# Kernel tuning notes

Hardware: AMD Instinct MI355X
Metric: run time of the kernel (lower is better)

The kernel has to match this reference:

```python
import jax, jax.numpy as jnp
import numpy as np

N_NODES = 100000
N_EDGES = 1600000
D = 64


def setup_inputs() -> dict:
    key = jax.random.key(0)
    k1, k2, k3, k4 = jax.random.split(key, 4)
    x = jax.random.normal(k1, (N_NODES, D), dtype=jnp.float32)
    # glorot-uniform scale for Linear weight [out_dim, in_dim]
    stdv = np.sqrt(6.0 / (D + D)).astype(np.float32)
    W = jax.random.uniform(k2, (D, D), dtype=jnp.float32, minval=-stdv, maxval=stdv)
    bias = jnp.zeros((D,), dtype=jnp.float32)  # forward() uses a zero bias
    edge_index = jax.random.randint(k3, (2, N_EDGES), 0, N_NODES, dtype=jnp.int64)
    counts = jax.random.randint(k4, (N_NODES,), 0, 16, dtype=jnp.int64)
    out_edge_index = jnp.arange(N_EDGES, dtype=jnp.int64)
    return {"x": x, "W": W, "bias": bias, "edge_index": edge_index,
            "counts": counts, "out_edge_index": out_edge_index, "layer_i": 0}


def reference(x, W, bias, edge_index, counts, out_edge_index, layer_i):
    # GCN layer: y = x @ W^T; gather by source; scatter-sum by destination; add bias.
    # counts / out_edge_index / layer_i are layout hints for the fused CUDA kernel
    # (mygraph.gcn) and do not change the math.
    y = x @ W.T                              # [N, D_out]
    src = edge_index[0]                      # [E]
    dst = edge_index[1]                      # [E]
    msgs = y[src]                            # [E, D_out] edge gather
    out = jax.ops.segment_sum(msgs, dst, num_segments=x.shape[0])  # [N, D_out]
    return out + bias
```

## Files before the change

### kernel.cpp

```cpp
#include <hip/hip_runtime.h>


#define DIM 64
#define BN 64
#define BN_SHIFT 6
#define BN_MASK 63
#define NB_MAX 2048
#define PB 256
#define CAPE 1536
#define OVF_MAX 262144

__device__ __forceinline__ unsigned short f32_to_bf16_rne(float f) {
    unsigned u = __float_as_uint(f);
    unsigned r = u + 0x7FFFu + ((u >> 16) & 1u);
    return (unsigned short)(r >> 16);
}

__global__ __launch_bounds__(1024) void fused_prep_kernel(
        const float* __restrict__ x, const int* __restrict__ ei,
        ushort4* __restrict__ xb4, int* __restrict__ gcnt,
        int* __restrict__ binned, int* __restrict__ ovf,
        int* __restrict__ ovfcnt, int E, int N, int nb, int total4) {
    __shared__ int h[NB_MAX];
    const int t = threadIdx.x;
    const int bid = blockIdx.x;

    for (int b = t; b < nb; b += 1024) h[b] = 0;
    __syncthreads();

    for (int i = bid * 1024 + t; i < total4; i += PB * 1024) {
        float4 v = ((const float4*)x)[i];
        ushort4 o;
        o.x = f32_to_bf16_rne(v.x); o.y = f32_to_bf16_rne(v.y);
        o.z = f32_to_bf16_rne(v.z); o.w = f32_to_bf16_rne(v.w);
        xb4[i] = o;
    }
    if (bid == 0 && t < 16) {
        ushort4 z; z.x = 0; z.y = 0; z.z = 0; z.w = 0;
        xb4[(size_t)N * 16 + t] = z;
    }

    for (int e = bid * 1024 + t; e < E; e += PB * 1024)
        atomicAdd(&h[ei[E + e] >> BN_SHIFT], 1);
    __syncthreads();

    for (int b = t; b < nb; b += 1024) {
        int c = h[b];
        int base = 0;
        if (c > 0) base = atomicAdd(&gcnt[b], c);
        h[b] = b * CAPE + base;
    }
    __syncthreads();

    for (int e = bid * 1024 + t; e < E; e += PB * 1024) {
        int s = ei[e];
        int d = ei[E + e];
        int b = d >> BN_SHIFT;
        int p = atomicAdd(&h[b], 1);
        if (p < b * CAPE + CAPE) {
            binned[p] = (s << BN_SHIFT) | (d & BN_MASK);
        } else {
            int q = atomicAdd(ovfcnt, 1);
            if (q < OVF_MAX) { ovf[2 * q] = s; ovf[2 * q + 1] = d; }
        }
    }
}

__device__ __forceinline__ void acc8(float (&a)[8], const uint4& v) {
    a[0] += __uint_as_float(v.x << 16); a[1] += __uint_as_float(v.x & 0xFFFF0000u);
    a[2] += __uint_as_float(v.y << 16); a[3] += __uint_as_float(v.y & 0xFFFF0000u);
    a[4] += __uint_as_float(v.z << 16); a[5] += __uint_as_float(v.z & 0xFFFF0000u);
    a[6] += __uint_as_float(v.w << 16); a[7] += __uint_as_float(v.w & 0xFFFF0000u);
}

__device__ __forceinline__ float epilogue64(const float (&a)[8],
                                            const float (&wv)[DIM], float bb) {
    float r0 = bb, r1 = 0.f, r2 = 0.f, r3 = 0.f;
    #pragma unroll
    for (int k = 0; k < DIM; k += 4) {
        r0 += __int_as_float(__builtin_amdgcn_readlane(
                  __float_as_int(a[(k + 0) & 7]), (k + 0) >> 3)) * wv[k + 0];
        r1 += __int_as_float(__builtin_amdgcn_readlane(
                  __float_as_int(a[(k + 1) & 7]), (k + 1) >> 3)) * wv[k + 1];
        r2 += __int_as_float(__builtin_amdgcn_readlane(
                  __float_as_int(a[(k + 2) & 7]), (k + 2) >> 3)) * wv[k + 2];
        r3 += __int_as_float(__builtin_amdgcn_readlane(
                  __float_as_int(a[(k + 3) & 7]), (k + 3) >> 3)) * wv[k + 3];
    }
    return (r0 + r1) + (r2 + r3);
}

__global__ __launch_bounds__(256) void sort_gather_kernel(
        const unsigned short* __restrict__ xh, const int* __restrict__ binned,
        const int* __restrict__ gcnt, const float* __restrict__ W,
        const float* __restrict__ bias, float* __restrict__ out, int N) {
    __shared__ int cnt[BN];
    __shared__ int basel[BN + 1];
    __shared__ int tmp[BN];
    __shared__ int slds[CAPE];

    const int t = threadIdx.x;
    const int g = blockIdx.x;
    const int lane = t & 63;
    const int wid = t >> 6;
    const int node0 = g << BN_SHIFT;

    float wv[DIM];
    #pragma unroll
    for (int k4 = 0; k4 < DIM / 4; ++k4) {
        float4 tw = *(const float4*)(W + (size_t)lane * DIM + k4 * 4);
        wv[k4 * 4 + 0] = tw.x; wv[k4 * 4 + 1] = tw.y;
        wv[k4 * 4 + 2] = tw.z; wv[k4 * 4 + 3] = tw.w;
    }
    const float bb = bias[lane];

    const int seg0 = g * CAPE;
    int len = gcnt[g];
    if (len > CAPE) len = CAPE;
    const int seg1 = seg0 + len;

    if (t < BN) cnt[t] = 0;
    __syncthreads();

    for (int i = seg0 + t; i < seg1; i += 256)
        atomicAdd(&cnt[binned[i] & BN_MASK], 1);
    __syncthreads();

    int myv = (t < BN) ? cnt[t] : 0;
    if (t < BN) tmp[t] = myv;
    __syncthreads();
    #pragma unroll
    for (int d = 1; d < BN; d <<= 1) {
        int u = (t < BN && t >= d) ? tmp[t - d] : 0;
        __syncthreads();
        if (t < BN) tmp[t] += u;
        __syncthreads();
    }
    if (t < BN) basel[t] = tmp[t] - myv;
    if (t == BN - 1) basel[BN] = tmp[t];
    if (t < BN) cnt[t] = tmp[t] - myv;
    __syncthreads();

    for (int i = seg0 + t; i < seg1; i += 256) {
        int v = binned[i];
        int p = atomicAdd(&cnt[v & BN_MASK], 1);
        slds[p] = v >> BN_SHIFT;
    }
    __syncthreads();

    const int sub8 = lane >> 3;
    const int fb   = (lane & 7) << 3;
    const int zrow = N;
    for (int q = wid; q < (BN >> 2); q += 4) {
        const int nl = q << 2;
        int b0 = basel[nl + 0], e0 = basel[nl + 1];
        int b1 = basel[nl + 1], e1 = basel[nl + 2];
        int b2 = basel[nl + 2], e2 = basel[nl + 3];
        int b3 = basel[nl + 3], e3 = basel[nl + 4];
        int c0 = (e0 - b0 + 7) >> 3, c1 = (e1 - b1 + 7) >> 3;
        int c2 = (e2 - b2 + 7) >> 3, c3 = (e3 - b3 + 7) >> 3;
        int cmax = max(max(c0, c1), max(c2, c3));
        cmax = __builtin_amdgcn_readfirstlane(cmax);

        float A0[8] = {0.f,0.f,0.f,0.f,0.f,0.f,0.f,0.f};
        float A1[8] = {0.f,0.f,0.f,0.f,0.f,0.f,0.f,0.f};
        float A2[8] = {0.f,0.f,0.f,0.f,0.f,0.f,0.f,0.f};
        float A3[8] = {0.f,0.f,0.f,0.f,0.f,0.f,0.f,0.f};

        for (int c = 0; c < cmax; ++c) {
            const int o = (c << 3) + sub8;
            int i0 = b0 + o, i1 = b1 + o, i2 = b2 + o, i3 = b3 + o;
            int s0 = slds[min(i0, CAPE - 1)];
            int s1 = slds[min(i1, CAPE - 1)];
            int s2 = slds[min(i2, CAPE - 1)];
            int s3 = slds[min(i3, CAPE - 1)];
            s0 = (i0 < e0) ? s0 : zrow;
            s1 = (i1 < e1) ? s1 : zrow;
            s2 = (i2 < e2) ? s2 : zrow;
            s3 = (i3 < e3) ? s3 : zrow;
            uint4 v0 = *(const uint4*)(xh + (size_t)s0 * DIM + fb);
            uint4 v1 = *(const uint4*)(xh + (size_t)s1 * DIM + fb);
            uint4 v2 = *(const uint4*)(xh + (size_t)s2 * DIM + fb);
            uint4 v3 = *(const uint4*)(xh + (size_t)s3 * DIM + fb);
            acc8(A0, v0); acc8(A1, v1); acc8(A2, v2); acc8(A3, v3);
        }

        #pragma unroll
        for (int d = 8; d <= 32; d <<= 1) {
            #pragma unroll
            for (int j = 0; j < 8; ++j) {
                A0[j] += __shfl_xor(A0[j], d, 64);
                A1[j] += __shfl_xor(A1[j], d, 64);
                A2[j] += __shfl_xor(A2[j], d, 64);
                A3[j] += __shfl_xor(A3[j], d, 64);
            }
        }

        const int n0 = node0 + nl;
        if (n0 + 0 < N) out[(size_t)(n0 + 0) * DIM + lane] = epilogue64(A0, wv, bb);
        if (n0 + 1 < N) out[(size_t)(n0 + 1) * DIM + lane] = epilogue64(A1, wv, bb);
        if (n0 + 2 < N) out[(size_t)(n0 + 2) * DIM + lane] = epilogue64(A2, wv, bb);
        if (n0 + 3 < N) out[(size_t)(n0 + 3) * DIM + lane] = epilogue64(A3, wv, bb);
    }
}

__global__ __launch_bounds__(256) void fixup_kernel(
        const float* __restrict__ x, const int* __restrict__ ovf,
        const int* __restrict__ ovfcnt, const float* __restrict__ W,
        float* __restrict__ out) {
    int cnt = *ovfcnt;
    if (cnt > OVF_MAX) cnt = OVF_MAX;
    if (cnt == 0) return;
    const int lane = threadIdx.x & 63;
    const int gwave = (blockIdx.x * blockDim.x + threadIdx.x) >> 6;
    const int total_waves = (gridDim.x * blockDim.x) >> 6;

    float wv[DIM];
    #pragma unroll
    for (int k4 = 0; k4 < DIM / 4; ++k4) {
        float4 tw = *(const float4*)(W + (size_t)lane * DIM + k4 * 4);
        wv[k4 * 4 + 0] = tw.x; wv[k4 * 4 + 1] = tw.y;
        wv[k4 * 4 + 2] = tw.z; wv[k4 * 4 + 3] = tw.w;
    }
    for (int i = gwave; i < cnt; i += total_waves) {
        int s = ovf[2 * i];
        int d = ovf[2 * i + 1];
        float v = x[(size_t)s * DIM + lane];
        float r0 = 0.f, r1 = 0.f, r2 = 0.f, r3 = 0.f;
        #pragma unroll
        for (int k = 0; k < DIM; k += 4) {
            r0 += __int_as_float(__builtin_amdgcn_readlane(__float_as_int(v), k + 0)) * wv[k + 0];
            r1 += __int_as_float(__builtin_amdgcn_readlane(__float_as_int(v), k + 1)) * wv[k + 1];
            r2 += __int_as_float(__builtin_amdgcn_readlane(__float_as_int(v), k + 2)) * wv[k + 2];
            r3 += __int_as_float(__builtin_amdgcn_readlane(__float_as_int(v), k + 3)) * wv[k + 3];
        }
        atomicAdd(&out[(size_t)d * DIM + lane], (r0 + r1) + (r2 + r3));
    }
}

__global__ void gcn_scatter_kernel(const float* __restrict__ x,
                                   const int* __restrict__ edge_index,
                                   float* __restrict__ out, int n_edges) {
    int gid = blockIdx.x * blockDim.x + threadIdx.x;
    int e = gid >> 4;
    if (e >= n_edges) return;
    int j = (gid & 15) << 2;
    int src = edge_index[e];
    int dst = edge_index[n_edges + e];
    const float4 v = *(const float4*)(x + (size_t)src * DIM + j);
    float* o = out + (size_t)dst * DIM + j;
    atomicAdd(o + 0, v.x); atomicAdd(o + 1, v.y);
    atomicAdd(o + 2, v.z); atomicAdd(o + 3, v.w);
}

__global__ void gcn_linear_inplace_kernel(float* __restrict__ out,
                                          const float* __restrict__ W,
                                          const float* __restrict__ bias,
                                          int n_nodes) {
    __shared__ float Wt[DIM * DIM];
    __shared__ float rows[4][DIM];
    int tid = threadIdx.x;
    int col = tid & 63;
    int r = tid >> 6;
    for (int i = tid; i < DIM * DIM; i += 256) {
        int c = i >> 6, k = i & 63;
        Wt[k * DIM + c] = W[i];
    }
    int row = blockIdx.x * 4 + r;
    if (row < n_nodes) rows[r][col] = out[(size_t)row * DIM + col];
    __syncthreads();
    if (row < n_nodes) {
        float a = 0.f;
        #pragma unroll
        for (int k = 0; k < DIM; ++k) a += rows[r][k] * Wt[k * DIM + col];
        out[(size_t)row * DIM + col] = a + bias[col];
    }
}

extern "C" void kernel_launch(void* const* d_in, const int* in_sizes, int n_in,
                              void* d_out, int out_size, void* d_ws, size_t ws_size,
                              hipStream_t stream) {
    const float* x          = (const float*)d_in[0];
    const float* W          = (const float*)d_in[1];
    const float* bias       = (const float*)d_in[2];
    const int*   edge_index = (const int*)d_in[3];

    const int E = in_sizes[3] / 2;
    const int N = in_sizes[0] / DIM;
    float* out = (float*)d_out;

    const int nb = (N + BN - 1) >> BN_SHIFT;

    auto align256 = [](size_t v) { return (v + 255) & ~(size_t)255; };
    const size_t xb_b   = align256(((size_t)N + 1) * DIM * 2);
    const size_t bin_b  = align256((size_t)nb * CAPE * 4);
    const size_t cnt_b  = align256(((size_t)nb + 64) * 4);
    const size_t ovf_b  = align256((size_t)OVF_MAX * 2 * 4);
    const size_t needA = xb_b + bin_b + cnt_b + ovf_b;

    if (nb <= NB_MAX && N < (1 << 24) && ws_size >= needA) {
        char* p = (char*)d_ws;
        ushort4* xb4 = (ushort4*)p;          p += xb_b;
        int* binned  = (int*)p;              p += bin_b;
        int* gcnt    = (int*)p;              p += cnt_b;
        int* ovf     = (int*)p;
        int* ovfcnt  = gcnt + nb;

        const int total4 = N * DIM / 4;

        hipMemsetAsync(gcnt, 0, cnt_b, stream);
        fused_prep_kernel<<<PB, 1024, 0, stream>>>(
            x, edge_index, xb4, gcnt, binned, ovf, ovfcnt, E, N, nb, total4);
        sort_gather_kernel<<<nb, 256, 0, stream>>>(
            (const unsigned short*)xb4, binned, gcnt, W, bias, out, N);
        fixup_kernel<<<64, 256, 0, stream>>>(x, ovf, ovfcnt, W, out);
    } else {
        hipMemsetAsync(d_out, 0, (size_t)out_size * sizeof(float), stream);
        long long total = (long long)E * 16;
        int grid = (int)((total + 255) / 256);
        gcn_scatter_kernel<<<grid, 256, 0, stream>>>(x, edge_index, out, E);
        int lgrid = (N + 3) / 4;
        gcn_linear_inplace_kernel<<<lgrid, 256, 0, stream>>>(out, W, bias, N);
    }
}
```

Measured before the change: 199.7 us.

## Cache edges in registers during binning and fold overflow fixup into gather kernel

Adds a prep kernel variant that loads each thread's edges once into registers (up to KMAX per thread) and reuses them for both the histogram and the scatter-to-bins pass. The x-to-bf16 conversion is placed between the two passes so its loads can overlap the LDS atomics. The separate fixup kernel is removed, and each gather block now scans the overflow list for edges whose destination falls in its bin and applies them with atomics. This saves one launch and the second read of edge_index. The cost is that every block reads the overflow count and has to scan the whole overflow list when it is non-empty, and the code keeps a dead epilogue64 call on a reinterpreted scalar.

Result: no change. 198.3 us (-0.7%).

```diff
diff --git a/kernel.cpp b/kernel.cpp
--- a/kernel.cpp
+++ b/kernel.cpp
@@ -7,6 +7,7 @@
 #define BN_MASK 63
 #define NB_MAX 2048
 #define PB 256
+#define KMAX 8
 #define CAPE 1536
 #define OVF_MAX 262144
 
@@ -14,6 +15,66 @@
     unsigned u = __float_as_uint(f);
     unsigned r = u + 0x7FFFu + ((u >> 16) & 1u);
     return (unsigned short)(r >> 16);
+}
+
+__global__ __launch_bounds__(1024) void fused_prep_reg_kernel(
+        const float* __restrict__ x, const int* __restrict__ ei,
+        ushort4* __restrict__ xb4, int* __restrict__ gcnt,
+        int* __restrict__ binned, int* __restrict__ ovf,
+        int* __restrict__ ovfcnt, int E, int N, int nb, int total4) {
+    __shared__ int h[NB_MAX];
+    const int t = threadIdx.x;
+    const int bid = blockIdx.x;
+
+    for (int b = t; b < nb; b += 1024) h[b] = 0;
+    __syncthreads();
+
+    int es[KMAX], ds[KMAX];
+    #pragma unroll
+    for (int k = 0; k < KMAX; ++k) {
+        int e = (k * PB + bid) * 1024 + t;
+        if (e < E) {
+            es[k] = ei[e];
+            ds[k] = ei[E + e];
+            atomicAdd(&h[ds[k] >> BN_SHIFT], 1);
+        } else {
+            ds[k] = -1;
+        }
+    }
+
+    for (int i = bid * 1024 + t; i < total4; i += PB * 1024) {
+        float4 v = ((const float4*)x)[i];
+        ushort4 o;
+        o.x = f32_to_bf16_rne(v.x); o.y = f32_to_bf16_rne(v.y);
+        o.z = f32_to_bf16_rne(v.z); o.w = f32_to_bf16_rne(v.w);
+        xb4[i] = o;
+    }
+    if (bid == 0 && t < 16) {
+        ushort4 z; z.x = 0; z.y = 0; z.z = 0; z.w = 0;
+        xb4[(size_t)N * 16 + t] = z;
+    }
+    __syncthreads();
+
+    for (int b = t; b < nb; b += 1024) {
+        int c = h[b];
+        int base = (c > 0) ? atomicAdd(&gcnt[b], c) : 0;
+        h[b] = b * CAPE + base;
+    }
+    __syncthreads();
+
+    #pragma unroll
+    for (int k = 0; k < KMAX; ++k) {
+        if (ds[k] >= 0) {
+            int b = ds[k] >> BN_SHIFT;
+            int p = atomicAdd(&h[b], 1);
+            if (p < b * CAPE + CAPE) {
+                binned[p] = (es[k] << BN_SHIFT) | (ds[k] & BN_MASK);
+            } else {
+                int q = atomicAdd(ovfcnt, 1);
+                if (q < OVF_MAX) { ovf[2 * q] = es[k]; ovf[2 * q + 1] = ds[k]; }
+            }
+        }
+    }
 }
 
 __global__ __launch_bounds__(1024) void fused_prep_kernel(
@@ -46,8 +107,7 @@
 
     for (int b = t; b < nb; b += 1024) {
         int c = h[b];
-        int base = 0;
-        if (c > 0) base = atomicAdd(&gcnt[b], c);
+        int base = (c > 0) ? atomicAdd(&gcnt[b], c) : 0;
         h[b] = b * CAPE + base;
     }
     __syncthreads();
@@ -91,9 +151,11 @@
 }
 
 __global__ __launch_bounds__(256) void sort_gather_kernel(
-        const unsigned short* __restrict__ xh, const int* __restrict__ binned,
-        const int* __restrict__ gcnt, const float* __restrict__ W,
-        const float* __restrict__ bias, float* __restrict__ out, int N) {
+        const unsigned short* __restrict__ xh, const float* __restrict__ xf,
+        const int* __restrict__ binned, const int* __restrict__ gcnt,
+        const int* __restrict__ ovf, const int* __restrict__ ovfcnt,
+        const float* __restrict__ W, const float* __restrict__ bias,
+        float* __restrict__ out, int N) {
     __shared__ int cnt[BN];
     __shared__ int basel[BN + 1];
     __shared__ int tmp[BN];
@@ -202,39 +264,29 @@
         if (n0 + 2 < N) out[(size_t)(n0 + 2) * DIM + lane] = epilogue64(A2, wv, bb);
         if (n0 + 3 < N) out[(size_t)(n0 + 3) * DIM + lane] = epilogue64(A3, wv, bb);
     }
-}
-
-__global__ __launch_bounds__(256) void fixup_kernel(
-        const float* __restrict__ x, const int* __restrict__ ovf,
-        const int* __restrict__ ovfcnt, const float* __restrict__ W,
-        float* __restrict__ out) {
-    int cnt = *ovfcnt;
-    if (cnt > OVF_MAX) cnt = OVF_MAX;
-    if (cnt == 0) return;
-    const int lane = threadIdx.x & 63;
-    const int gwave = (blockIdx.x * blockDim.x + threadIdx.x) >> 6;
-    const int total_waves = (gridDim.x * blockDim.x) >> 6;
-
-    float wv[DIM];
-    #pragma unroll
-    for (int k4 = 0; k4 < DIM / 4; ++k4) {
-        float4 tw = *(const float4*)(W + (size_t)lane * DIM + k4 * 4);
-        wv[k4 * 4 + 0] = tw.x; wv[k4 * 4 + 1] = tw.y;
-        wv[k4 * 4 + 2] = tw.z; wv[k4 * 4 + 3] = tw.w;
-    }
-    for (int i = gwave; i < cnt; i += total_waves) {
-        int s = ovf[2 * i];
-        int d = ovf[2 * i + 1];
-        float v = x[(size_t)s * DIM + lane];
-        float r0 = 0.f, r1 = 0.f, r2 = 0.f, r3 = 0.f;
-        #pragma unroll
-        for (int k = 0; k < DIM; k += 4) {
-            r0 += __int_as_float(__builtin_amdgcn_readlane(__float_as_int(v), k + 0)) * wv[k + 0];
-            r1 += __int_as_float(__builtin_amdgcn_readlane(__float_as_int(v), k + 1)) * wv[k + 1];
-            r2 += __int_as_float(__builtin_amdgcn_readlane(__float_as_int(v), k + 2)) * wv[k + 2];
-            r3 += __int_as_float(__builtin_amdgcn_readlane(__float_as_int(v), k + 3)) * wv[k + 3];
-        }
-        atomicAdd(&out[(size_t)d * DIM + lane], (r0 + r1) + (r2 + r3));
+
+    __syncthreads();
+    int oc = *ovfcnt;
+    if (oc > 0) {
+        if (oc > OVF_MAX) oc = OVF_MAX;
+        for (int i = wid; i < oc; i += 4) {
+            int s = ovf[2 * i];
+            int d = ovf[2 * i + 1];
+            if ((d >> BN_SHIFT) == g) {
+                float v = xf[(size_t)s * DIM + lane];
+                float r = epilogue64(*(const float(*)[8])&v, wv, 0.f);
+                float rr0 = 0.f, rr1 = 0.f, rr2 = 0.f, rr3 = 0.f;
+                #pragma unroll
+                for (int k = 0; k < DIM; k += 4) {
+                    rr0 += __int_as_float(__builtin_amdgcn_readlane(__float_as_int(v), k + 0)) * wv[k + 0];
+                    rr1 += __int_as_float(__builtin_amdgcn_readlane(__float_as_int(v), k + 1)) * wv[k + 1];
+                    rr2 += __int_as_float(__builtin_amdgcn_readlane(__float_as_int(v), k + 2)) * wv[k + 2];
+                    rr3 += __int_as_float(__builtin_amdgcn_readlane(__float_as_int(v), k + 3)) * wv[k + 3];
+                }
+                (void)r;
+                atomicAdd(&out[(size_t)d * DIM + lane], (rr0 + rr1) + (rr2 + rr3));
+            }
+        }
     }
 }
 
@@ -309,11 +361,16 @@
         const int total4 = N * DIM / 4;
 
         hipMemsetAsync(gcnt, 0, cnt_b, stream);
-        fused_prep_kernel<<<PB, 1024, 0, stream>>>(
-            x, edge_index, xb4, gcnt, binned, ovf, ovfcnt, E, N, nb, total4);
+        if ((long long)E <= (long long)PB * 1024 * KMAX) {
+            fused_prep_reg_kernel<<<PB, 1024, 0, stream>>>(
+                x, edge_index, xb4, gcnt, binned, ovf, ovfcnt, E, N, nb, total4);
+        } else {
+            fused_prep_kernel<<<PB, 1024, 0, stream>>>(
+                x, edge_index, xb4, gcnt, binned, ovf, ovfcnt, E, N, nb, total4);
+        }
         sort_gather_kernel<<<nb, 256, 0, stream>>>(
-            (const unsigned short*)xb4, binned, gcnt, W, bias, out, N);
-        fixup_kernel<<<64, 256, 0, stream>>>(x, ovf, ovfcnt, W, out);
+            (const unsigned short*)xb4, x, binned, gcnt, ovf, ovfcnt,
+            W, bias, out, N);
     } else {
         hipMemsetAsync(d_out, 0, (size_t)out_size * sizeof(float), stream);
         long long total = (long long)E * 16;
```
